# Kernel tuning notes

Hardware: AMD Instinct MI355X
Metric: run time of the kernel (lower is better)

## Reference

```python
import jax, jax.numpy as jnp
import numpy as np
import math

B, S, DIM = 2, 2048, 2048
H, KV = 32, 8
HD = DIM // H          # 64
REP = H // KV          # 4
NEG = -1e9


def setup_inputs() -> dict:
    key = jax.random.key(0)
    ks = jax.random.split(key, 8)
    x = jax.random.normal(ks[0], (B, S, DIM), dtype=jnp.float32)
    # RoPE frequencies: theta = 10000^{-2i/d}, angles = pos * theta
    inv_freq = 1.0 / (10000.0 ** (jnp.arange(0, HD, 2, dtype=jnp.float32) / HD))  # [HD/2]
    angles = jnp.arange(S, dtype=jnp.float32)[:, None] * inv_freq[None, :]        # [S, HD/2]
    freqs_cos = jnp.cos(angles)
    freqs_sin = jnp.sin(angles)
    # additive causal mask [1,1,S,S]
    causal = jnp.tril(jnp.ones((S, S), dtype=bool))
    mask = jnp.where(causal, 0.0, NEG).astype(jnp.float32)[None, None]
    sc = 1.0 / math.sqrt(DIM)
    wq = jax.random.normal(ks[1], (DIM, H * HD), dtype=jnp.float32) * sc
    wk = jax.random.normal(ks[2], (DIM, KV * HD), dtype=jnp.float32) * sc
    wv = jax.random.normal(ks[3], (DIM, KV * HD), dtype=jnp.float32) * sc
    wo = jax.random.normal(ks[4], (H * HD, DIM), dtype=jnp.float32) * sc
    return {"x": x, "freqs_cos": freqs_cos, "freqs_sin": freqs_sin,
            "mask": mask, "wq": wq, "wk": wk, "wv": wv, "wo": wo}


def _rope(t, cos, sin):
    # t: [B,S,nh,HD]; interleaved (even, odd) pairs == view_as_complex layout
    te, to = t[..., 0::2], t[..., 1::2]
    c = cos[None, :, None, :]  # [1,S,1,HD/2]
    s = sin[None, :, None, :]
    oe = te * c - to * s
    oo = te * s + to * c
    return jnp.stack([oe, oo], axis=-1).reshape(t.shape)


def reference(x, freqs_cos, freqs_sin, mask, wq, wk, wv, wo):
    b, s, _ = x.shape
    q = (x @ wq).reshape(b, s, H, HD)
    k = (x @ wk).reshape(b, s, KV, HD)
    v = (x @ wv).reshape(b, s, KV, HD)
    q = _rope(q, freqs_cos, freqs_sin)
    k = _rope(k, freqs_cos, freqs_sin)
    # GQA without materializing repeat_interleave: group q heads by kv head
    # repeat_interleave maps query head h -> kv head h // REP
    qg = q.transpose(0, 2, 1, 3).reshape(b, KV, REP, s, HD)  # [B,KV,REP,S,HD]
    kg = k.transpose(0, 2, 1, 3)                              # [B,KV,S,HD]
    vg = v.transpose(0, 2, 1, 3)
    scores = jnp.einsum('bgrqd,bgkd->bgrqk', qg, kg) / math.sqrt(HD)
    scores = scores + mask[:, :, None]                        # [1,1,1,S,S] broadcast
    attn = jax.nn.softmax(scores, axis=-1)
    out = jnp.einsum('bgrqk,bgkd->bgrqd', attn, vg)           # [B,KV,REP,S,HD]
    out = out.reshape(b, H, s, HD).transpose(0, 2, 1, 3).reshape(b, s, H * HD)
    return out @ wo
```

## Files before the change

### kernel.cpp

```cpp
#include <hip/hip_runtime.h>
#include <hip/hip_bf16.h>

#define B_ 2
#define S_ 2048
#define DIM_ 2048
#define H_ 32
#define KV_ 8
#define HD_ 64

typedef __bf16 bf16x8 __attribute__((ext_vector_type(8)));
typedef __bf16 bf16x4 __attribute__((ext_vector_type(4)));
typedef float f32x4 __attribute__((ext_vector_type(4)));
typedef float f32x16 __attribute__((ext_vector_type(16)));
typedef unsigned u32x2 __attribute__((ext_vector_type(2)));

#define GLOAD16(gp, lp) __builtin_amdgcn_global_load_lds( \
    (const __attribute__((address_space(1))) void*)(gp),  \
    (__attribute__((address_space(3))) void*)(lp), 16, 0, 0)

__global__ __launch_bounds__(256) void prep_all(const float* __restrict__ x,
                                                __bf16* __restrict__ x_bf, int n4,
                                                const float* __restrict__ wq,
                                                const float* __restrict__ wk,
                                                const float* __restrict__ wv,
                                                const float* __restrict__ wo,
                                                __bf16* __restrict__ wqkv_t,
                                                __bf16* __restrict__ wo_t) {
    if (blockIdx.z == 2) {
        const int nb = 64 * 96;
        const int blin = blockIdx.y * 64 + blockIdx.x;
        for (int i = blin * 256 + threadIdx.x; i < n4; i += nb * 256) {
            float4 v = ((const float4*)x)[i];
            bf16x4 o;
            o[0] = (__bf16)v.x; o[1] = (__bf16)v.y; o[2] = (__bf16)v.z; o[3] = (__bf16)v.w;
            ((bf16x4*)x_bf)[i] = o;
        }
        return;
    }
    __shared__ float t[32][33];
    const int bk = blockIdx.x * 32, bn = blockIdx.y * 32;
    const int tx = threadIdx.x & 31, ty = threadIdx.x >> 5;
    const float* W; __bf16* Wt; int N, src;
    if (blockIdx.z == 0) {
        Wt = wqkv_t;
        if (bn < 2048)      { W = wq; N = 2048; src = bn; }
        else if (bn < 2560) { W = wk; N = 512;  src = bn - 2048; }
        else                { W = wv; N = 512;  src = bn - 2560; }
    } else {
        if (bn >= 2048) return;
        Wt = wo_t; W = wo; N = 2048; src = bn;
    }
#pragma unroll
    for (int i = 0; i < 4; i++)
        t[ty * 4 + i][tx] = W[(size_t)(bk + ty * 4 + i) * N + src + tx];
    __syncthreads();
#pragma unroll
    for (int i = 0; i < 4; i++)
        Wt[(size_t)(bn + ty * 4 + i) * 2048 + bk + tx] = (__bf16)t[tx][ty * 4 + i];
}

__global__ __launch_bounds__(512, 4)
void gemm256_qkv(const __bf16* __restrict__ A, const __bf16* __restrict__ Bt,
                 __bf16* __restrict__ q_bf, __bf16* __restrict__ k_bf,
                 __bf16* __restrict__ vt_bf,
                 const float* __restrict__ fc, const float* __restrict__ fs) {
    __shared__ __align__(16) char smem[81920];
    char* lA = smem;
    char* lB = smem + 32768;
    const int K = DIM_;
    const int tid = threadIdx.x, lane = tid & 63, wid = tid >> 6;
    const int wr2 = wid >> 2, wc2 = wid & 3;
    const int fr = lane & 15, fg = lane >> 4;
    const int id = blockIdx.x;
    const long i0 = (long)(id >> 4) * 128;
    const long j0 = (long)(id & 15) * 192;

    const int r0 = tid >> 3;
    const int cc = ((tid & 7) ^ (r0 & 7)) * 8;
    const __bf16* pA = A + (i0 + r0) * (long)K + cc;
    const __bf16* pB = Bt + (j0 + r0) * (long)K + cc;
    const int NT = K >> 6;

    f32x4 acc[4][3] = {};

#define STG(kt, buf) do { \
    GLOAD16(pA + (long)(kt) * 64,                  lA + (buf) * 16384 + tid * 16); \
    GLOAD16(pA + (long)64 * K + (long)(kt) * 64,   lA + (buf) * 16384 + 8192 + tid * 16); \
    GLOAD16(pB + (long)(kt) * 64,                  lB + (buf) * 24576 + tid * 16); \
    GLOAD16(pB + (long)64 * K + (long)(kt) * 64,   lB + (buf) * 24576 + 8192 + tid * 16); \
    GLOAD16(pB + (long)128 * K + (long)(kt) * 64,  lB + (buf) * 24576 + 16384 + tid * 16); } while (0)

    STG(0, 0);

    for (int kt = 0; kt < NT; ++kt) {
        const int cur = kt & 1, nxt = cur ^ 1;
        const bool nl = (kt + 1 < NT);
        const char* cA = lA + cur * 16384;
        const char* cB = lB + cur * 24576;

        if (nl) STG(kt + 1, nxt);
        if (nl) asm volatile("s_waitcnt vmcnt(5)" ::: "memory");
        else    asm volatile("s_waitcnt vmcnt(0)" ::: "memory");
        __builtin_amdgcn_s_barrier();
        asm volatile("" ::: "memory");

        bf16x8 af[4], bfv[3];
#pragma unroll
        for (int ks = 0; ks < 2; ks++) {
#pragma unroll
            for (int nf = 0; nf < 3; nf++) {
                int row = wc2 * 48 + nf * 16 + fr;
                bfv[nf] = *(const bf16x8*)(cB + row * 128 + (((ks << 2) | fg) ^ (row & 7)) * 16);
            }
#pragma unroll
            for (int mf = 0; mf < 4; mf++) {
                int row = wr2 * 64 + mf * 16 + fr;
                af[mf] = *(const bf16x8*)(cA + row * 128 + (((ks << 2) | fg) ^ (row & 7)) * 16);
            }
            __builtin_amdgcn_s_setprio(1);
#pragma unroll
            for (int mf = 0; mf < 4; mf++)
#pragma unroll
                for (int nf = 0; nf < 3; nf++)
                    acc[mf][nf] = __builtin_amdgcn_mfma_f32_16x16x32_bf16(af[mf], bfv[nf], acc[mf][nf], 0, 0, 0);
            __builtin_amdgcn_s_setprio(0);
        }
        __builtin_amdgcn_s_barrier();
    }
#undef STG

#pragma unroll
    for (int mf = 0; mf < 4; mf++)
#pragma unroll
        for (int nf = 0; nf < 3; nf++) {
            const long colf = j0 + wc2 * 48 + nf * 16;
            const long col = colf + fr;
            const long row0 = i0 + wr2 * 64 + mf * 16 + fg * 4;
            if (colf < 2048) {
#pragma unroll
                for (int j = 0; j < 4; j++)
                    q_bf[(row0 + j) * 2048 + col] = (__bf16)acc[mf][nf][j];
            } else if (colf < 2560) {
                const int kd = (int)(col - 2048);
                const int i_ = (kd & 63) >> 1;
                const float sgn = (fr & 1) ? 1.0f : -1.0f;
#pragma unroll
                for (int j = 0; j < 4; j++) {
                    long row = row0 + j;
                    int s = (int)(row & (S_ - 1));
                    float cv = fc[s * 32 + i_], sv = fs[s * 32 + i_];
                    float v = acc[mf][nf][j];
                    float p = __shfl_xor(v, 1, 64);
                    k_bf[row * 512 + kd] = (__bf16)(v * cv + sgn * sv * p);
                }
            } else {
                const int vd = (int)(col - 2560);
                int b = (int)(row0 >> 11);
                int s = (int)(row0 & (S_ - 1));
                bf16x4 pk;
#pragma unroll
                for (int j = 0; j < 4; j++) pk[j] = (__bf16)acc[mf][nf][j];
                *(bf16x4*)(vt_bf + ((size_t)(b * KV_ + (vd >> 6)) * HD_ + (vd & 63)) * S_ + s) = pk;
            }
        }
}

__global__ __launch_bounds__(512, 2)
void gemm256_o(const __bf16* __restrict__ A, const __bf16* __restrict__ Bt,
               float* __restrict__ C) {
    __shared__ __align__(16) char smem[98304];
    char* lA = smem;
    char* lB = smem + 32768;
    const int K = DIM_;
    const int tid = threadIdx.x, lane = tid & 63, wid = tid >> 6;
    const int wr2 = wid >> 2, wc2 = wid & 3;
    const int fr = lane & 15, fg = lane >> 4;
    const int id = blockIdx.x;
    const long i0 = (long)(id >> 3) * 128;
    const long j0 = (long)(id & 7) * 256;

    const int r0 = tid >> 3;
    const int cc = ((tid & 7) ^ (r0 & 7)) * 8;
    const __bf16* pA = A + (i0 + r0) * (long)K + cc;
    const __bf16* pB = Bt + (j0 + r0) * (long)K + cc;
    const int NT = K >> 6;

    f32x4 acc[4][4] = {};

#define STG(kt, buf) do { \
    GLOAD16(pA + (long)(kt) * 64,                  lA + (buf) * 16384 + tid * 16); \
    GLOAD16(pA + (long)64 * K + (long)(kt) * 64,   lA + (buf) * 16384 + 8192 + tid * 16); \
    GLOAD16(pB + (long)(kt) * 64,                  lB + (buf) * 32768 + tid * 16); \
    GLOAD16(pB + (long)64 * K + (long)(kt) * 64,   lB + (buf) * 32768 + 8192 + tid * 16); \
    GLOAD16(pB + (long)128 * K + (long)(kt) * 64,  lB + (buf) * 32768 + 16384 + tid * 16); \
    GLOAD16(pB + (long)192 * K + (long)(kt) * 64,  lB + (buf) * 32768 + 24576 + tid * 16); } while (0)

    STG(0, 0);

    for (int kt = 0; kt < NT; ++kt) {
        const int cur = kt & 1, nxt = cur ^ 1;
        const bool nl = (kt + 1 < NT);
        const char* cA = lA + cur * 16384;
        const char* cB = lB + cur * 32768;

        if (nl) STG(kt + 1, nxt);
        if (nl) asm volatile("s_waitcnt vmcnt(6)" ::: "memory");
        else    asm volatile("s_waitcnt vmcnt(0)" ::: "memory");
        __builtin_amdgcn_s_barrier();
        asm volatile("" ::: "memory");

        bf16x8 af[4], bfv[4];
#pragma unroll
        for (int ks = 0; ks < 2; ks++) {
#pragma unroll
            for (int nf = 0; nf < 4; nf++) {
                int row = wc2 * 64 + nf * 16 + fr;
                bfv[nf] = *(const bf16x8*)(cB + row * 128 + (((ks << 2) | fg) ^ (row & 7)) * 16);
            }
#pragma unroll
            for (int mf = 0; mf < 4; mf++) {
                int row = wr2 * 64 + mf * 16 + fr;
                af[mf] = *(const bf16x8*)(cA + row * 128 + (((ks << 2) | fg) ^ (row & 7)) * 16);
            }
            __builtin_amdgcn_s_setprio(1);
#pragma unroll
            for (int mf = 0; mf < 4; mf++)
#pragma unroll
                for (int nf = 0; nf < 4; nf++)
                    acc[mf][nf] = __builtin_amdgcn_mfma_f32_16x16x32_bf16(af[mf], bfv[nf], acc[mf][nf], 0, 0, 0);
            __builtin_amdgcn_s_setprio(0);
        }
        __builtin_amdgcn_s_barrier();
    }
#undef STG

#pragma unroll
    for (int mf = 0; mf < 4; mf++)
#pragma unroll
        for (int nf = 0; nf < 4; nf++)
#pragma unroll
            for (int j = 0; j < 4; j++) {
                long row = i0 + wr2 * 64 + mf * 16 + fg * 4 + j;
                long col = j0 + wc2 * 64 + nf * 16 + fr;
                C[row * 2048 + col] = acc[mf][nf][j];
            }
}

__global__ __launch_bounds__(256, 4)
void attn_fwd(const __bf16* __restrict__ Q, const __bf16* __restrict__ Kb,
              const __bf16* __restrict__ Vt, __bf16* __restrict__ O,
              const float* __restrict__ fc, const float* __restrict__ fs) {
    extern __shared__ __align__(16) char smem[];
    __bf16* lK  = (__bf16*)smem;
    __bf16* lVt = (__bf16*)(smem + 16384);

    const int tid = threadIdx.x;
    const int lane = tid & 63;
    const int wid = tid >> 6;
    const int ln = lane & 31;
    const int hi = lane >> 5;

    const int id = blockIdx.x;
    const int round = id >> 8;
    const int q4 = (id >> 6) & 3;
    const int inner = id & 63;
    const int g = inner & 7;
    const int hb = inner >> 3;
    const int b = hb & 1;
    const int h = g * 4 + (hb >> 1);
    const int chunk = (round == 0) ? 12 + q4
                    : (round == 1) ? 3 - q4
                    : (round == 2) ? 8 + q4
                    :                7 - q4;
    const int QS = H_ * HD_, KS = KV_ * HD_;
    const float K2 = 0.18033688011112042f;
    const float mK = 8.0f * K2;

    const __bf16* Kbse = Kb + (size_t)(b * S_) * KS + g * HD_;
    const __bf16* Vbse = Vt + (size_t)((b * KV_ + g) * HD_) * S_;

    bf16x8 onesf;
#pragma unroll
    for (int j = 0; j < 8; j++) onesf[j] = (__bf16)1.0f;

    const int c0 = tid, c1 = tid + 256;
    const int kr0 = c0 & 63, kd0 = c0 >> 6;
    const int kr1 = c1 & 63, kd1 = c1 >> 6;
    const __bf16* Ksrc0 = Kbse + (size_t)kr0 * KS + kd0 * 8;
    const __bf16* Ksrc1 = Kbse + (size_t)kr1 * KS + kd1 * 8;
    const __bf16* Vsrc0 = Vbse + (size_t)kr0 * S_ + kd0 * 8;
    const __bf16* Vsrc1 = Vbse + (size_t)kr1 * S_ + kd1 * 8;

    auto stage = [&](int t, int buf) {
        GLOAD16(Ksrc0 + (size_t)t * 64 * KS, lK + buf * 4096 + c0 * 8);
        GLOAD16(Ksrc1 + (size_t)t * 64 * KS, lK + buf * 4096 + c1 * 8);
        GLOAD16(Vsrc0 + t * 64,              lVt + buf * 4096 + c0 * 8);
        GLOAD16(Vsrc1 + t * 64,              lVt + buf * 4096 + c1 * 8);
    };

    const int q0w = chunk * 128 + wid * 32;
    const int qrow = q0w + ln;
    const int nt = 2 * chunk + 2;
    const int nkv_w = (q0w >> 6) + 1;

    const __bf16* Qb = Q + (size_t)(b * S_ + qrow) * QS + h * HD_;
    const float* cz = fc + (size_t)qrow * 32;
    const float* sz = fs + (size_t)qrow * 32;
    bf16x8 qf[4];
#pragma unroll
    for (int kk = 0; kk < 4; kk++) {
        bf16x8 raw = *(const bf16x8*)(Qb + kk * 16 + hi * 8);
#pragma unroll
        for (int p = 0; p < 4; p++) {
            const int i = kk * 8 + hi * 4 + p;
            float cv = cz[i], sv = sz[i];
            float e = (float)raw[2 * p], o = (float)raw[2 * p + 1];
            qf[kk][2 * p]     = (__bf16)(e * cv - o * sv);
            qf[kk][2 * p + 1] = (__bf16)(e * sv + o * cv);
        }
    }

    f32x16 o0 = {}, o1 = {}, o2 = {};

    stage(0, 0);

    for (int t = 0; t < nt; t++) {
        if (t + 1 < nt) {
            stage(t + 1, (t + 1) & 1);
            asm volatile("s_waitcnt vmcnt(4)" ::: "memory");
        } else {
            asm volatile("s_waitcnt vmcnt(0)" ::: "memory");
        }
        __builtin_amdgcn_s_barrier();
        asm volatile("" ::: "memory");
        if (t < nkv_w) {
            const char* lKc = (const char*)(lK + (t & 1) * 4096);
            const char* lVc = (const char*)(lVt + (t & 1) * 4096);
            const int p0 = t * 64;

            f32x16 s0 = {}, s1 = {};
            __builtin_amdgcn_s_setprio(1);
#pragma unroll
            for (int kk = 0; kk < 4; kk++) {
                bf16x8 ka = *(const bf16x8*)(lKc + (kk * 2 + hi) * 1024 + ln * 16);
                s0 = __builtin_amdgcn_mfma_f32_32x32x16_bf16(ka, qf[kk], s0, 0, 0, 0);
            }
#pragma unroll
            for (int kk = 0; kk < 4; kk++) {
                bf16x8 ka = *(const bf16x8*)(lKc + (kk * 2 + hi) * 1024 + (32 + ln) * 16);
                s1 = __builtin_amdgcn_mfma_f32_32x32x16_bf16(ka, qf[kk], s1, 0, 0, 0);
            }
            __builtin_amdgcn_s_setprio(0);

            if (t == nkv_w - 1) {
#pragma unroll
                for (int rr = 0; rr < 16; rr++) {
                    int crow = (rr & 3) + 8 * (rr >> 2) + 4 * hi;
                    if (p0 + crow > qrow)      s0[rr] = -1e30f;
                    if (p0 + 32 + crow > qrow) s1[rr] = -1e30f;
                }
            }

#pragma unroll
            for (int rr = 0; rr < 16; rr++) {
                s0[rr] = exp2f(s0[rr] * K2 - mK);
                s1[rr] = exp2f(s1[rr] * K2 - mK);
            }

            __builtin_amdgcn_s_setprio(1);
#pragma unroll
            for (int c = 0; c < 2; c++) {
                const f32x16& pe = c ? s1 : s0;
                unsigned w[4][2];
#pragma unroll
                for (int gi = 0; gi < 4; gi++)
#pragma unroll
                    for (int p = 0; p < 2; p++) {
                        unsigned short lo = __builtin_bit_cast(unsigned short, (__bf16)pe[4 * gi + 2 * p]);
                        unsigned short hp = __builtin_bit_cast(unsigned short, (__bf16)pe[4 * gi + 2 * p + 1]);
                        w[gi][p] = (unsigned)lo | ((unsigned)hp << 16);
                    }
                unsigned pw0[4], pw1[4];
#pragma unroll
                for (int p = 0; p < 2; p++) {
                    u32x2 ra = __builtin_amdgcn_permlane32_swap(w[0][p], w[1][p], false, false);
                    pw0[p] = ra[0]; pw0[2 + p] = ra[1];
                    u32x2 rb = __builtin_amdgcn_permlane32_swap(w[2][p], w[3][p], false, false);
                    pw1[p] = rb[0]; pw1[2 + p] = rb[1];
                }
                bf16x8 pa0 = __builtin_bit_cast(bf16x8, *(uint4*)pw0);
                bf16x8 pa1 = __builtin_bit_cast(bf16x8, *(uint4*)pw1);
#pragma unroll
                for (int half = 0; half < 2; half++) {
                    const int ks = 2 * c + half;
                    bf16x8 pa = half ? pa1 : pa0;
                    bf16x8 va0 = *(const bf16x8*)(lVc + (ks * 2 + hi) * 1024 + ln * 16);
                    bf16x8 va1 = *(const bf16x8*)(lVc + (ks * 2 + hi) * 1024 + (32 + ln) * 16);
                    o0 = __builtin_amdgcn_mfma_f32_32x32x16_bf16(va0, pa, o0, 0, 0, 0);
                    o1 = __builtin_amdgcn_mfma_f32_32x32x16_bf16(va1, pa, o1, 0, 0, 0);
                    o2 = __builtin_amdgcn_mfma_f32_32x32x16_bf16(onesf, pa, o2, 0, 0, 0);
                }
            }
            __builtin_amdgcn_s_setprio(0);
        }
        __builtin_amdgcn_s_barrier();
    }

    const float inv = 1.0f / o2[0];
    __bf16* Oq = O + (size_t)(b * S_ + qrow) * QS + h * HD_;
#pragma unroll
    for (int db = 0; db < 2; db++) {
        const f32x16& oo = db ? o1 : o0;
#pragma unroll
        for (int gi = 0; gi < 4; gi++) {
            bf16x4 pk;
#pragma unroll
            for (int j = 0; j < 4; j++) pk[j] = (__bf16)(oo[4 * gi + j] * inv);
            *(bf16x4*)(Oq + db * 32 + 8 * gi + 4 * hi) = pk;
        }
    }
}

extern "C" void kernel_launch(void* const* d_in, const int* in_sizes, int n_in,
                              void* d_out, int out_size, void* d_ws, size_t ws_size,
                              hipStream_t stream) {
    const float* x  = (const float*)d_in[0];
    const float* fc = (const float*)d_in[1];
    const float* fs = (const float*)d_in[2];
    const float* wq = (const float*)d_in[4];
    const float* wk = (const float*)d_in[5];
    const float* wv = (const float*)d_in[6];
    const float* wo = (const float*)d_in[7];
    float* out = (float*)d_out;

    const size_t N0 = (size_t)B_ * S_ * DIM_;
    const size_t N1 = (size_t)B_ * S_ * H_ * HD_;
    const size_t N2 = (size_t)B_ * S_ * KV_ * HD_;
    const size_t N3 = (size_t)DIM_ * H_ * HD_;
    const size_t N4 = (size_t)DIM_ * KV_ * HD_;

    __bf16* x_bf = (__bf16*)d_ws;
    __bf16* q_bf = x_bf + N0;
    __bf16* k_bf = q_bf + N1;
    __bf16* vt_bf = k_bf + N2;
    __bf16* wqkv_t = vt_bf + N2;
    __bf16* wo_t = wqkv_t + N3 + 2 * N4;
    __bf16* ao_bf = x_bf;

    prep_all<<<dim3(64, 96, 3), 256, 0, stream>>>(x, x_bf, (int)(N0 / 4),
                                                  wq, wk, wv, wo, wqkv_t, wo_t);

    gemm256_qkv<<<dim3(512), 512, 0, stream>>>(x_bf, wqkv_t, q_bf, k_bf, vt_bf, fc, fs);

    attn_fwd<<<dim3(1024), 256, 32768, stream>>>(q_bf, k_bf, vt_bf, ao_bf, fc, fs);

    gemm256_o<<<dim3(256), 512, 0, stream>>>(ao_bf, wo_t, out);
}
```

Measured before the change: 186.1 us.

## Widen attention blocks to 8 waves over 256-query chunks

```diff
diff --git a/kernel.cpp b/kernel.cpp
--- a/kernel.cpp
+++ b/kernel.cpp
@@ -246,7 +246,7 @@
             }
 }
 
-__global__ __launch_bounds__(256, 4)
+__global__ __launch_bounds__(512, 4)
 void attn_fwd(const __bf16* __restrict__ Q, const __bf16* __restrict__ Kb,
               const __bf16* __restrict__ Vt, __bf16* __restrict__ O,
               const float* __restrict__ fc, const float* __restrict__ fs) {
@@ -261,17 +261,13 @@
     const int hi = lane >> 5;
 
     const int id = blockIdx.x;
-    const int round = id >> 8;
-    const int q4 = (id >> 6) & 3;
-    const int inner = id & 63;
-    const int g = inner & 7;
-    const int hb = inner >> 3;
-    const int b = hb & 1;
-    const int h = g * 4 + (hb >> 1);
-    const int chunk = (round == 0) ? 12 + q4
-                    : (round == 1) ? 3 - q4
-                    : (round == 2) ? 8 + q4
-                    :                7 - q4;
+    const int g = id & 7;
+    const int c3 = (id >> 3) & 7;
+    const int h2 = (id >> 6) & 3;
+    const int round = (id >> 8) & 1;
+    const int b = round;
+    const int h = g * 4 + h2;
+    const int chunk = round ? c3 : 7 - c3;
     const int QS = H_ * HD_, KS = KV_ * HD_;
     const float K2 = 0.18033688011112042f;
     const float mK = 8.0f * K2;
@@ -283,24 +279,18 @@
 #pragma unroll
     for (int j = 0; j < 8; j++) onesf[j] = (__bf16)1.0f;
 
-    const int c0 = tid, c1 = tid + 256;
-    const int kr0 = c0 & 63, kd0 = c0 >> 6;
-    const int kr1 = c1 & 63, kd1 = c1 >> 6;
+    const int kr0 = tid & 63, kd0 = tid >> 6;
     const __bf16* Ksrc0 = Kbse + (size_t)kr0 * KS + kd0 * 8;
-    const __bf16* Ksrc1 = Kbse + (size_t)kr1 * KS + kd1 * 8;
     const __bf16* Vsrc0 = Vbse + (size_t)kr0 * S_ + kd0 * 8;
-    const __bf16* Vsrc1 = Vbse + (size_t)kr1 * S_ + kd1 * 8;
 
     auto stage = [&](int t, int buf) {
-        GLOAD16(Ksrc0 + (size_t)t * 64 * KS, lK + buf * 4096 + c0 * 8);
-        GLOAD16(Ksrc1 + (size_t)t * 64 * KS, lK + buf * 4096 + c1 * 8);
-        GLOAD16(Vsrc0 + t * 64,              lVt + buf * 4096 + c0 * 8);
-        GLOAD16(Vsrc1 + t * 64,              lVt + buf * 4096 + c1 * 8);
+        GLOAD16(Ksrc0 + (size_t)t * 64 * KS, lK + buf * 4096 + tid * 8);
+        GLOAD16(Vsrc0 + t * 64,              lVt + buf * 4096 + tid * 8);
     };
 
-    const int q0w = chunk * 128 + wid * 32;
+    const int q0w = chunk * 256 + wid * 32;
     const int qrow = q0w + ln;
-    const int nt = 2 * chunk + 2;
+    const int nt = chunk * 4 + 4;
     const int nkv_w = (q0w >> 6) + 1;
 
     const __bf16* Qb = Q + (size_t)(b * S_ + qrow) * QS + h * HD_;
@@ -327,7 +317,7 @@
     for (int t = 0; t < nt; t++) {
         if (t + 1 < nt) {
             stage(t + 1, (t + 1) & 1);
-            asm volatile("s_waitcnt vmcnt(4)" ::: "memory");
+            asm volatile("s_waitcnt vmcnt(2)" ::: "memory");
         } else {
             asm volatile("s_waitcnt vmcnt(0)" ::: "memory");
         }
@@ -452,7 +442,7 @@
 
     gemm256_qkv<<<dim3(512), 512, 0, stream>>>(x_bf, wqkv_t, q_bf, k_bf, vt_bf, fc, fs);
 
-    attn_fwd<<<dim3(1024), 256, 32768, stream>>>(q_bf, k_bf, vt_bf, ao_bf, fc, fs);
+    attn_fwd<<<dim3(512), 512, 32768, stream>>>(q_bf, k_bf, vt_bf, ao_bf, fc, fs);
 
     gemm256_o<<<dim3(256), 512, 0, stream>>>(ao_bf, wo_t, out);
 }
```

Result: slower. 190.4 us (+2.3%).
